# Optimization experiments

Measured on AMD Instinct MI355X. Metric: run time of the kernel, lower is better.

The kernel has to match this reference:

```python
import jax, jax.numpy as jnp
import numpy as np

N_USER = 50000
N_ITEM = 50000
E = 600000
IN_F = 128
HID = 256
OUT = 256
HEADS = 4
D = HID // HEADS
EPS = 1e-5


def setup_inputs() -> dict:
    key = jax.random.key(0)
    ks = jax.random.split(key, 32)
    inp = {}
    inp['x_user'] = jax.random.normal(ks[0], (N_USER, IN_F), jnp.float32)
    inp['x_item'] = jax.random.normal(ks[1], (N_ITEM, IN_F), jnp.float32)
    inp['ui_src'] = jax.random.randint(ks[2], (E,), 0, N_USER)
    inp['ui_dst'] = jax.random.randint(ks[3], (E,), 0, N_ITEM)
    inp['iu_src'] = jax.random.randint(ks[4], (E,), 0, N_ITEM)
    inp['iu_dst'] = jax.random.randint(ks[5], (E,), 0, N_USER)
    dims = [IN_F, HID, HID, HID]
    i = 6
    for l in range(4):
        din = dims[l]
        inp['W%d' % (l + 1)] = jax.random.normal(ks[i], (2, din, HID), jnp.float32) * (1.0 / np.sqrt(din)); i += 1
        inp['al%d' % (l + 1)] = jax.random.normal(ks[i], (2, HEADS, D), jnp.float32) * 0.1; i += 1
        inp['ar%d' % (l + 1)] = jax.random.normal(ks[i], (2, HEADS, D), jnp.float32) * 0.1; i += 1
        inp['b%d' % (l + 1)] = jnp.zeros((2, HID), jnp.float32); i += 1
    inp['bn_g'] = jnp.ones((3, 2, HID), jnp.float32)
    inp['bn_b'] = jnp.zeros((3, 2, HID), jnp.float32)
    return inp


def gat_conv(x_src, x_dst, src, dst, W, al, ar, b, n_dst):
    # DGL GATConv: shared fc, per-head additive attention, segment softmax over dst.
    H, Dh = al.shape
    z_src = (x_src @ W).reshape(-1, H, Dh)   # [Ns,H,D]
    z_dst = (x_dst @ W).reshape(-1, H, Dh)   # [Nd,H,D]
    el = jnp.sum(z_src * al, axis=-1)        # [Ns,H]
    er = jnp.sum(z_dst * ar, axis=-1)        # [Nd,H]
    e = jax.nn.leaky_relu(el[src] + er[dst], 0.2)          # [E,H]
    m = jax.ops.segment_max(e, dst, num_segments=n_dst)    # [Nd,H]
    ex = jnp.exp(e - m[dst])
    s = jax.ops.segment_sum(ex, dst, num_segments=n_dst)
    alpha = ex / s[dst]                                    # [E,H]
    out = jax.ops.segment_sum(z_src[src] * alpha[:, :, None], dst, num_segments=n_dst)
    return out.reshape(n_dst, H * Dh) + b


def batchnorm(x, g, beta):
    mu = jnp.mean(x, axis=0)
    var = jnp.mean((x - mu) ** 2, axis=0)
    return (x - mu) * jax.lax.rsqrt(var + EPS) * g + beta


def _forward(x_user, x_item, ui_src, ui_dst, iu_src, iu_dst,
             W1, al1, ar1, b1, W2, al2, ar2, b2, W3, al3, ar3, b3, W4, al4, ar4, b4,
             bn_g, bn_b):
    def layer(hu, hi, W, al, ar, b):
        h_item = gat_conv(hu, hi, ui_src, ui_dst, W[0], al[0], ar[0], b[0], N_ITEM)
        h_user = gat_conv(hi, hu, iu_src, iu_dst, W[1], al[1], ar[1], b[1], N_USER)
        return h_user, h_item  # mean over single relation per dst type = identity

    hu, hi = layer(x_user, x_item, W1, al1, ar1, b1)
    hu = jax.nn.leaky_relu(batchnorm(hu, bn_g[0, 0], bn_b[0, 0]), 0.01)
    hi = jax.nn.leaky_relu(batchnorm(hi, bn_g[0, 1], bn_b[0, 1]), 0.01)
    hu, hi = layer(hu, hi, W2, al2, ar2, b2)
    hu = jax.nn.leaky_relu(batchnorm(hu, bn_g[1, 0], bn_b[1, 0]), 0.01)
    hi = jax.nn.leaky_relu(batchnorm(hi, bn_g[1, 1], bn_b[1, 1]), 0.01)
    hu, hi = layer(hu, hi, W3, al3, ar3, b3)
    hu = jnp.tanh(batchnorm(hu, bn_g[2, 0], bn_b[2, 0]))
    hi = jnp.tanh(batchnorm(hi, bn_g[2, 1], bn_b[2, 1]))
    hu, hi = layer(hu, hi, W4, al4, ar4, b4)
    return hu.reshape(-1, OUT), hi.reshape(-1, OUT)


def reference(x_user, x_item, ui_src, ui_dst, iu_src, iu_dst,
              W1, al1, ar1, b1, W2, al2, ar2, b2, W3, al3, ar3, b3, W4, al4, ar4, b4,
              bn_g, bn_b):
    return _forward(x_user, x_item, ui_src, ui_dst, iu_src, iu_dst,
                    W1, al1, ar1, b1, W2, al2, ar2, b2, W3, al3, ar3, b3,
                    W4, al4, ar4, b4, bn_g, bn_b)
```

## Files before the change

### kernel.cpp

```cpp
#include <hip/hip_runtime.h>
#include <hip/hip_bf16.h>
#include <type_traits>

#define NN 50000
#define NE 600000
#define HF 256

typedef float f32x4 __attribute__((ext_vector_type(4)));
typedef _Float16 f16x8 __attribute__((ext_vector_type(8)));
typedef _Float16 f16x4 __attribute__((ext_vector_type(4)));

__global__ __launch_bounds__(256) void k_tofp16_2(const float* __restrict__ A,
                                                  const float* __restrict__ B,
                                                  _Float16* __restrict__ OA,
                                                  _Float16* __restrict__ OB, int n4) {
  int i = blockIdx.x * 256 + threadIdx.x;
  const float* X = (i < n4) ? A : B;
  _Float16* Y = (i < n4) ? OA : OB;
  int j = (i < n4) ? i : i - n4;
  if (j < n4) {
    float4 v = reinterpret_cast<const float4*>(X)[j];
    f16x4 o = {(_Float16)v.x, (_Float16)v.y, (_Float16)v.z, (_Float16)v.w};
    reinterpret_cast<f16x4*>(Y)[j] = o;
  }
}

struct TArgs {
  const float* W[8];
  _Float16* dst[8];
  int K[8];
  int cum[9];
};
__global__ __launch_bounds__(256) void k_transpose_all(TArgs t) {
  int idx = blockIdx.x * 256 + threadIdx.x;
#pragma unroll
  for (int s = 0; s < 8; ++s) {
    if (idx >= t.cum[s] && idx < t.cum[s + 1]) {
      int local = idx - t.cum[s];
      int K = t.K[s];
      int k = local >> 8;
      int n = local & 255;
      t.dst[s][(size_t)n * K + k] = (_Float16)t.W[s][local];
    }
  }
}

__global__ __launch_bounds__(256) void k_makeattn_all(
    const float* __restrict__ W1, const float* __restrict__ W2,
    const float* __restrict__ W3, const float* __restrict__ W4,
    const float* __restrict__ ar1, const float* __restrict__ ar2,
    const float* __restrict__ ar3, const float* __restrict__ ar4,
    float* __restrict__ out) {
  int idx = blockIdx.x * 256 + threadIdx.x;
  if (idx >= 8 * 256 * 4) return;
  int h = idx & 3;
  int k = (idx >> 2) & 255;
  int s = idx >> 10;
  int l = s >> 1, r = s & 1;
  int K = (l == 0) ? 128 : 256;
  if (k >= K) return;
  const float* W = (l == 0 ? W1 : l == 1 ? W2 : l == 2 ? W3 : W4) + (size_t)r * K * 256;
  const float* a = (l == 0 ? ar1 : l == 1 ? ar2 : l == 2 ? ar3 : ar4) + r * 256 + h * 64;
  const float* wrow = W + (size_t)k * 256 + h * 64;
  float sum = 0.f;
#pragma unroll 8
  for (int d = 0; d < 64; ++d) sum += wrow[d] * a[d];
  out[s * 1024 + k * 4 + h] = sum;
}

__global__ __launch_bounds__(256) void k_gemv_er2(const _Float16* __restrict__ Xi,
                                                  const _Float16* __restrict__ Xu,
                                                  const float* __restrict__ war0,
                                                  const float* __restrict__ war1,
                                                  float* __restrict__ ER0, float* __restrict__ ER1,
                                                  int K) {
  int nb = (NN + 3) / 4;
  int rel = blockIdx.x >= nb;
  int bid = rel ? blockIdx.x - nb : blockIdx.x;
  const _Float16* X = rel ? Xu : Xi;
  const float* wa = rel ? war1 : war0;
  float* out = rel ? ER1 : ER0;
  int wid = bid * 4 + (threadIdx.x >> 6);
  if (wid >= NN) return;
  int lane = threadIdx.x & 63;
  float p0 = 0.f, p1 = 0.f, p2 = 0.f, p3 = 0.f;
  int k0 = lane * 4;
  if (k0 < K) {
    f16x4 x = *reinterpret_cast<const f16x4*>(X + (size_t)wid * K + k0);
    float xv[4] = {(float)x.x, (float)x.y, (float)x.z, (float)x.w};
#pragma unroll
    for (int j = 0; j < 4; ++j) {
      float4 wv = *reinterpret_cast<const float4*>(wa + (k0 + j) * 4);
      p0 += xv[j] * wv.x; p1 += xv[j] * wv.y; p2 += xv[j] * wv.z; p3 += xv[j] * wv.w;
    }
  }
#pragma unroll
  for (int off = 32; off > 0; off >>= 1) {
    p0 += __shfl_down(p0, off); p1 += __shfl_down(p1, off);
    p2 += __shfl_down(p2, off); p3 += __shfl_down(p3, off);
  }
  if (lane == 0)
    *reinterpret_cast<float4*>(out + (size_t)wid * 4) = (float4){p0, p1, p2, p3};
}

struct GArgs {
  const _Float16* A0; const _Float16* A1;
  const _Float16* Wt0; const _Float16* Wt1;
  _Float16* Z0; _Float16* Z1;
  const float* al0; const float* al1;
  float* EL0; float* EL1;
  int M, K;
};

__global__ __launch_bounds__(256) void k_gemm5(GArgs ga) {
  __shared__ _Float16 As[2][64 * 64];
  const int nrow = (NN + 63) / 64;
  int side = blockIdx.x >= nrow;
  int bid = side ? blockIdx.x - nrow : blockIdx.x;
  const _Float16* A = side ? ga.A1 : ga.A0;
  const _Float16* Wt = side ? ga.Wt1 : ga.Wt0;
  _Float16* Z = side ? ga.Z1 : ga.Z0;
  const float* al = side ? ga.al1 : ga.al0;
  float* EL = side ? ga.EL1 : ga.EL0;
  const int K = ga.K, M = ga.M;
  int row0 = bid * 64;
  int wave = threadIdx.x >> 6;
  int lane = threadIdx.x & 63;
  int lr = lane & 15, kg = lane >> 4;
  int col0 = wave * 64;

  auto stage = [&](int buf, int k0) {
#pragma unroll
    for (int j = 0; j < 2; ++j) {
      int Lb = j * 4096 + wave * 1024;
      int L = Lb + lane * 16;
      int r = L >> 7;
      int kb = (L & 127) ^ ((r & 7) << 4);
      int rg = row0 + r; rg = rg < M ? rg : M - 1;
      const char* gsrc = (const char*)A + ((size_t)rg * K + k0) * 2 + kb;
      char* ldst = (char*)(&As[buf][0]) + Lb;
      __builtin_amdgcn_global_load_lds(
          (const __attribute__((address_space(1))) unsigned int*)gsrc,
          (__attribute__((address_space(3))) unsigned int*)ldst, 16, 0, 0);
    }
  };

  f32x4 acc[4][4];
#pragma unroll
  for (int i = 0; i < 4; ++i)
#pragma unroll
    for (int j = 0; j < 4; ++j) acc[i][j] = (f32x4){0.f, 0.f, 0.f, 0.f};

  int nt = K >> 6;
  stage(0, 0);
  __syncthreads();
  for (int t = 0; t < nt; ++t) {
    if (t + 1 < nt) stage((t + 1) & 1, (t + 1) * 64);
    const char* abuf = (const char*)(&As[t & 1][0]);
#pragma unroll
    for (int s = 0; s < 2; ++s) {
      int kk = t * 64 + s * 32 + kg * 8;
      f16x8 af[4], bfr[4];
#pragma unroll
      for (int mt = 0; mt < 4; ++mt) {
        int r = mt * 16 + lr;
        int cb = ((s << 6) | (kg << 4)) ^ ((r & 7) << 4);
        af[mt] = *reinterpret_cast<const f16x8*>(abuf + r * 128 + cb);
      }
#pragma unroll
      for (int ct = 0; ct < 4; ++ct) {
        int c = col0 + ct * 16 + lr;
        bfr[ct] = *reinterpret_cast<const f16x8*>(Wt + (size_t)c * K + kk);
      }
#pragma unroll
      for (int mt = 0; mt < 4; ++mt)
#pragma unroll
        for (int ct = 0; ct < 4; ++ct)
          acc[mt][ct] = __builtin_amdgcn_mfma_f32_16x16x32_f16(af[mt], bfr[ct], acc[mt][ct], 0, 0, 0);
    }
    __syncthreads();
  }

#pragma unroll
  for (int mt = 0; mt < 4; ++mt) {
#pragma unroll
    for (int r = 0; r < 4; ++r) {
      int row = row0 + mt * 16 + kg * 4 + r;
      if (row < M) {
#pragma unroll
        for (int ct = 0; ct < 4; ++ct) {
          int col = col0 + ct * 16 + lr;
          Z[(size_t)row * HF + col] = (_Float16)acc[mt][ct][r];
        }
      }
    }
  }
  float al4[4];
#pragma unroll
  for (int ct = 0; ct < 4; ++ct) al4[ct] = al[col0 + ct * 16 + lr];
#pragma unroll
  for (int mt = 0; mt < 4; ++mt) {
#pragma unroll
    for (int r = 0; r < 4; ++r) {
      float p = acc[mt][0][r] * al4[0] + acc[mt][1][r] * al4[1] +
                acc[mt][2][r] * al4[2] + acc[mt][3][r] * al4[3];
#pragma unroll
      for (int off = 1; off < 16; off <<= 1) p += __shfl_xor(p, off);
      int row = row0 + mt * 16 + kg * 4 + r;
      if (lr == 0 && row < M) EL[(size_t)row * 4 + wave] = p;
    }
  }
}

__global__ __launch_bounds__(256) void k_hist2(const int* __restrict__ d0, const int* __restrict__ d1,
                                               int* __restrict__ c0, int* __restrict__ c1) {
  int t = blockIdx.x * 256 + threadIdx.x;
  if (t < NE) atomicAdd(&c0[d0[t]], 1);
  else if (t < 2 * NE) atomicAdd(&c1[d1[t - NE]], 1);
}

__global__ __launch_bounds__(1024) void k_scan1_2(const int* __restrict__ c0, const int* __restrict__ c1,
                                                  int* __restrict__ rp0, int* __restrict__ rp1,
                                                  int* __restrict__ b0, int* __restrict__ b1, int nscan) {
  __shared__ int tmp[1024];
  int rel = blockIdx.x >= nscan;
  int blk = rel ? blockIdx.x - nscan : blockIdx.x;
  const int* counts = rel ? c1 : c0;
  int* rp = rel ? rp1 : rp0;
  int* bsum = rel ? b1 : b0;
  int i = blk * 1024 + threadIdx.x;
  int v = (i < NN) ? counts[i] : 0;
  tmp[threadIdx.x] = v;
  __syncthreads();
  for (int off = 1; off < 1024; off <<= 1) {
    int t = (threadIdx.x >= off) ? tmp[threadIdx.x - off] : 0;
    __syncthreads();
    tmp[threadIdx.x] += t;
    __syncthreads();
  }
  if (i < NN) rp[i] = tmp[threadIdx.x] - v;
  if (threadIdx.x == 1023) bsum[blk] = tmp[1023];
}

__global__ __launch_bounds__(128) void k_scan2_2(int* __restrict__ b0, int* __restrict__ b1, int nb) {
  int rel = threadIdx.x >> 6;
  int l = threadIdx.x & 63;
  int* bsum = rel ? b1 : b0;
  int orig = (l < nb) ? bsum[l] : 0;
  int v = orig;
#pragma unroll
  for (int off = 1; off < 64; off <<= 1) {
    int t = __shfl_up(v, off);
    if (l >= off) v += t;
  }
  if (l < nb) bsum[l] = v - orig;
}

__global__ __launch_bounds__(1024) void k_scan3_2(int* __restrict__ rp0, int* __restrict__ rp1,
                                                  const int* __restrict__ b0, const int* __restrict__ b1,
                                                  int nscan) {
  int rel = blockIdx.x >= nscan;
  int blk = rel ? blockIdx.x - nscan : blockIdx.x;
  int* rp = rel ? rp1 : rp0;
  const int* bsum = rel ? b1 : b0;
  int i = blk * 1024 + threadIdx.x;
  if (i < NN) rp[i] += bsum[blk];
  if (i == 0) rp[NN] = NE;
}

__global__ __launch_bounds__(256) void k_scatter2(
    const int* __restrict__ s0, const int* __restrict__ d0,
    const int* __restrict__ s1, const int* __restrict__ d1,
    const int* __restrict__ rp0, const int* __restrict__ rp1,
    int* __restrict__ f0, int* __restrict__ f1,
    int* __restrict__ cs0, int* __restrict__ cs1) {
  int t = blockIdx.x * 256 + threadIdx.x;
  if (t < NE) {
    int d = d0[t];
    int pos = rp0[d] + atomicAdd(&f0[d], 1);
    cs0[pos] = s0[t];
  } else if (t < 2 * NE) {
    int e = t - NE;
    int d = d1[e];
    int pos = rp1[d] + atomicAdd(&f1[d], 1);
    cs1[pos] = s1[e];
  }
}

__device__ __forceinline__ float pick_h(float4 v, int h) {
  float r = v.x;
  r = (h == 1) ? v.y : r;
  r = (h == 2) ? v.z : r;
  r = (h == 3) ? v.w : r;
  return r;
}

template <typename OT>
__global__ __launch_bounds__(256) void k_agg2(
    const int* __restrict__ rpA, const int* __restrict__ csA,
    const float* __restrict__ elA, const float* __restrict__ erA,
    const _Float16* __restrict__ ZA, const float* __restrict__ bA, OT* __restrict__ oA,
    const int* __restrict__ rpB, const int* __restrict__ csB,
    const float* __restrict__ elB, const float* __restrict__ erB,
    const _Float16* __restrict__ ZB, const float* __restrict__ bB, OT* __restrict__ oB) {
  __shared__ float exs[4][256];
  __shared__ int ssrc[4][64];
  int nb = (NN + 3) / 4;
  int rel = blockIdx.x >= nb;
  int bid = rel ? blockIdx.x - nb : blockIdx.x;
  const int* rp = rel ? rpB : rpA;
  const int* csrc = rel ? csB : csA;
  const float* el = rel ? elB : elA;
  const float* er = rel ? erB : erA;
  const _Float16* Z = rel ? ZB : ZA;
  const float* bias = rel ? bB : bA;
  OT* out = rel ? oB : oA;

  int wv = threadIdx.x >> 6;
  int wid = bid * 4 + wv;
  if (wid >= NN) return;
  int lane = threadIdx.x & 63;
  int half = lane >> 5, l5 = lane & 31;
  int c0 = l5 * 8;
  int h = l5 >> 3;
  int beg = rp[wid], end = rp[wid + 1];
  int deg = end - beg;

  if (deg == 0) {
    if (half == 0) {
      float4 b0 = *reinterpret_cast<const float4*>(bias + c0);
      float4 b1 = *reinterpret_cast<const float4*>(bias + c0 + 4);
      if constexpr (std::is_same<OT, float>::value) {
        float4* op = reinterpret_cast<float4*>(out + (size_t)wid * HF + c0);
        op[0] = b0; op[1] = b1;
      } else {
        f16x8 o = {(_Float16)b0.x, (_Float16)b0.y, (_Float16)b0.z, (_Float16)b0.w,
                   (_Float16)b1.x, (_Float16)b1.y, (_Float16)b1.z, (_Float16)b1.w};
        *reinterpret_cast<f16x8*>(out + (size_t)wid * HF + c0) = o;
      }
    }
    return;
  }

  if (deg <= 64) {
    int s = 0;
    float4 x = {-1e30f, -1e30f, -1e30f, -1e30f};
    float4 b = *reinterpret_cast<const float4*>(er + (size_t)wid * 4);
    if (lane < deg) {
      s = csrc[beg + lane];
      float4 a = reinterpret_cast<const float4*>(el)[s];
      x.x = a.x + b.x; x.x = x.x >= 0.f ? x.x : 0.2f * x.x;
      x.y = a.y + b.y; x.y = x.y >= 0.f ? x.y : 0.2f * x.y;
      x.z = a.z + b.z; x.z = x.z >= 0.f ? x.z : 0.2f * x.z;
      x.w = a.w + b.w; x.w = x.w >= 0.f ? x.w : 0.2f * x.w;
    }
    float4 m = x;
#pragma unroll
    for (int off = 32; off > 0; off >>= 1) {
      m.x = fmaxf(m.x, __shfl_xor(m.x, off));
      m.y = fmaxf(m.y, __shfl_xor(m.y, off));
      m.z = fmaxf(m.z, __shfl_xor(m.z, off));
      m.w = fmaxf(m.w, __shfl_xor(m.w, off));
    }
    float4 ex = {0.f, 0.f, 0.f, 0.f};
    if (lane < deg) {
      ex.x = __expf(x.x - m.x);
      ex.y = __expf(x.y - m.y);
      ex.z = __expf(x.z - m.z);
      ex.w = __expf(x.w - m.w);
    }
    float4 sm = ex;
#pragma unroll
    for (int off = 32; off > 0; off >>= 1) {
      sm.x += __shfl_xor(sm.x, off);
      sm.y += __shfl_xor(sm.y, off);
      sm.z += __shfl_xor(sm.z, off);
      sm.w += __shfl_xor(sm.w, off);
    }
    float inv = 1.0f / pick_h(sm, h);
    if (lane < deg) {
      *reinterpret_cast<float4*>(&exs[wv][lane * 4]) = ex;
      ssrc[wv][lane] = s;
    }
    float a8[8] = {0.f, 0.f, 0.f, 0.f, 0.f, 0.f, 0.f, 0.f};
    int j = half;
#define AGG_STEP(J)                                                        \
    {                                                                      \
      int sj = ssrc[wv][(J)];                                              \
      float wj = exs[wv][(J) * 4 + h];                                     \
      f16x8 z = *reinterpret_cast<const f16x8*>(Z + (size_t)sj * HF + c0); \
      _Pragma("unroll")                                                    \
      for (int q = 0; q < 8; ++q) a8[q] += wj * (float)z[q];               \
    }
    for (; j + 6 < deg; j += 8) {
      AGG_STEP(j); AGG_STEP(j + 2); AGG_STEP(j + 4); AGG_STEP(j + 6);
    }
    for (; j < deg; j += 2) { AGG_STEP(j); }
#undef AGG_STEP
#pragma unroll
    for (int q = 0; q < 8; ++q) a8[q] += __shfl_xor(a8[q], 32);
    if (half == 0) {
      float4 b0 = *reinterpret_cast<const float4*>(bias + c0);
      float4 b1 = *reinterpret_cast<const float4*>(bias + c0 + 4);
      float r0 = a8[0] * inv + b0.x, r1 = a8[1] * inv + b0.y;
      float r2 = a8[2] * inv + b0.z, r3 = a8[3] * inv + b0.w;
      float r4 = a8[4] * inv + b1.x, r5 = a8[5] * inv + b1.y;
      float r6 = a8[6] * inv + b1.z, r7 = a8[7] * inv + b1.w;
      if constexpr (std::is_same<OT, float>::value) {
        float4* op = reinterpret_cast<float4*>(out + (size_t)wid * HF + c0);
        op[0] = (float4){r0, r1, r2, r3};
        op[1] = (float4){r4, r5, r6, r7};
      } else {
        f16x8 o = {(_Float16)r0, (_Float16)r1, (_Float16)r2, (_Float16)r3,
                   (_Float16)r4, (_Float16)r5, (_Float16)r6, (_Float16)r7};
        *reinterpret_cast<f16x8*>(out + (size_t)wid * HF + c0) = o;
      }
    }
    return;
  }

  {
    int c4 = lane * 4;
    int h4 = lane >> 4;
    float4 b = *reinterpret_cast<const float4*>(er + (size_t)wid * 4);
    float4 m = {-1e30f, -1e30f, -1e30f, -1e30f};
    for (int e = beg; e < end; ++e) {
      int s = csrc[e];
      float4 a = reinterpret_cast<const float4*>(el)[s];
      float4 x;
      x.x = a.x + b.x; x.x = x.x >= 0.f ? x.x : 0.2f * x.x;
      x.y = a.y + b.y; x.y = x.y >= 0.f ? x.y : 0.2f * x.y;
      x.z = a.z + b.z; x.z = x.z >= 0.f ? x.z : 0.2f * x.z;
      x.w = a.w + b.w; x.w = x.w >= 0.f ? x.w : 0.2f * x.w;
      m.x = fmaxf(m.x, x.x); m.y = fmaxf(m.y, x.y);
      m.z = fmaxf(m.z, x.z); m.w = fmaxf(m.w, x.w);
    }
    float4 sm = {0.f, 0.f, 0.f, 0.f};
    float4 acc = {0.f, 0.f, 0.f, 0.f};
    for (int e = beg; e < end; ++e) {
      int s = csrc[e];
      float4 a = reinterpret_cast<const float4*>(el)[s];
      float4 x;
      x.x = a.x + b.x; x.x = x.x >= 0.f ? x.x : 0.2f * x.x;
      x.y = a.y + b.y; x.y = x.y >= 0.f ? x.y : 0.2f * x.y;
      x.z = a.z + b.z; x.z = x.z >= 0.f ? x.z : 0.2f * x.z;
      x.w = a.w + b.w; x.w = x.w >= 0.f ? x.w : 0.2f * x.w;
      float4 exv;
      exv.x = __expf(x.x - m.x); exv.y = __expf(x.y - m.y);
      exv.z = __expf(x.z - m.z); exv.w = __expf(x.w - m.w);
      sm.x += exv.x; sm.y += exv.y; sm.z += exv.z; sm.w += exv.w;
      float w0 = pick_h(exv, h4);
      f16x4 z0 = *reinterpret_cast<const f16x4*>(Z + (size_t)s * HF + c4);
      acc.x += w0 * (float)z0.x;
      acc.y += w0 * (float)z0.y;
      acc.z += w0 * (float)z0.z;
      acc.w += w0 * (float)z0.w;
    }
    float inv = 1.0f / pick_h(sm, h4);
    float4 bv = *reinterpret_cast<const float4*>(bias + c4);
    float r0 = acc.x * inv + bv.x, r1 = acc.y * inv + bv.y;
    float r2 = acc.z * inv + bv.z, r3 = acc.w * inv + bv.w;
    if constexpr (std::is_same<OT, float>::value) {
      *reinterpret_cast<float4*>(out + (size_t)wid * HF + c4) = (float4){r0, r1, r2, r3};
    } else {
      f16x4 o = {(_Float16)r0, (_Float16)r1, (_Float16)r2, (_Float16)r3};
      *reinterpret_cast<f16x4*>(out + (size_t)wid * HF + c4) = o;
    }
  }
}

__global__ __launch_bounds__(256) void k_bn_stats2(const _Float16* __restrict__ XU,
                                                   const _Float16* __restrict__ XI,
                                                   float* __restrict__ su, float* __restrict__ qu,
                                                   float* __restrict__ si, float* __restrict__ qi) {
  int rel = blockIdx.x >> 9;
  int blk = blockIdx.x & 511;
  const _Float16* X = rel ? XI : XU;
  float* sums = rel ? si : su;
  float* sqs = rel ? qi : qu;
  int c = threadIdx.x;
  float s = 0.f, q = 0.f;
  for (int r = blk; r < NN; r += 512) {
    float v = (float)X[(size_t)r * HF + c];
    s += v;
    q += v * v;
  }
  atomicAdd(&sums[c], s);
  atomicAdd(&sqs[c], q);
}

__global__ __launch_bounds__(256) void k_bn_apply2(
    const _Float16* __restrict__ XU, const _Float16* __restrict__ XI,
    const float* __restrict__ su, const float* __restrict__ qu,
    const float* __restrict__ si, const float* __restrict__ qi,
    const float* __restrict__ gU, const float* __restrict__ btU,
    const float* __restrict__ gI, const float* __restrict__ btI,
    _Float16* __restrict__ YU, _Float16* __restrict__ YI, int act) {
  const int nb = NN * HF / 8 / 256;
  int rel = blockIdx.x >= nb;
  int bid = rel ? blockIdx.x - nb : blockIdx.x;
  const _Float16* X = rel ? XI : XU;
  const float* sums = rel ? si : su;
  const float* sqs = rel ? qi : qu;
  const float* g = rel ? gI : gU;
  const float* bt = rel ? btI : btU;
  _Float16* Y = rel ? YI : YU;
  int gid = bid * 256 + threadIdx.x;
  int i0 = gid * 8;
  int c0 = i0 & 255;
  const float invN = 1.0f / NN;
  f16x8 xv = *reinterpret_cast<const f16x8*>(X + i0);
  float4 s0 = *reinterpret_cast<const float4*>(sums + c0);
  float4 s1 = *reinterpret_cast<const float4*>(sums + c0 + 4);
  float4 q0 = *reinterpret_cast<const float4*>(sqs + c0);
  float4 q1 = *reinterpret_cast<const float4*>(sqs + c0 + 4);
  float4 g0 = *reinterpret_cast<const float4*>(g + c0);
  float4 g1 = *reinterpret_cast<const float4*>(g + c0 + 4);
  float4 b0 = *reinterpret_cast<const float4*>(bt + c0);
  float4 b1 = *reinterpret_cast<const float4*>(bt + c0 + 4);
  float sa[8] = {s0.x, s0.y, s0.z, s0.w, s1.x, s1.y, s1.z, s1.w};
  float qa[8] = {q0.x, q0.y, q0.z, q0.w, q1.x, q1.y, q1.z, q1.w};
  float ga[8] = {g0.x, g0.y, g0.z, g0.w, g1.x, g1.y, g1.z, g1.w};
  float ba[8] = {b0.x, b0.y, b0.z, b0.w, b1.x, b1.y, b1.z, b1.w};
  f16x8 o;
#pragma unroll
  for (int j = 0; j < 8; ++j) {
    float mu = sa[j] * invN;
    float var = qa[j] * invN - mu * mu;
    float sc = rsqrtf(var + 1e-5f) * ga[j];
    float v = ((float)xv[j] - mu) * sc + ba[j];
    v = act ? tanhf(v) : (v >= 0.f ? v : 0.01f * v);
    o[j] = (_Float16)v;
  }
  *reinterpret_cast<f16x8*>(Y + i0) = o;
}

extern "C" void kernel_launch(void* const* d_in, const int* in_sizes, int n_in,
                              void* d_out, int out_size, void* d_ws, size_t ws_size,
                              hipStream_t stream) {
  (void)in_sizes; (void)n_in; (void)out_size; (void)ws_size;
  const float* x_user = (const float*)d_in[0];
  const float* x_item = (const float*)d_in[1];
  const int* ui_src = (const int*)d_in[2];
  const int* ui_dst = (const int*)d_in[3];
  const int* iu_src = (const int*)d_in[4];
  const int* iu_dst = (const int*)d_in[5];
  const float *Wp[4], *alp[4], *arp[4], *bp[4];
  for (int l = 0; l < 4; ++l) {
    Wp[l]  = (const float*)d_in[6 + 4 * l];
    alp[l] = (const float*)d_in[7 + 4 * l];
    arp[l] = (const float*)d_in[8 + 4 * l];
    bp[l]  = (const float*)d_in[9 + 4 * l];
  }
  const float* bng = (const float*)d_in[22];
  const float* bnb = (const float*)d_in[23];

  char* w = (char*)d_ws;
  auto alloc = [&](size_t bytes) -> void* {
    void* p = (void*)w;
    w += (bytes + 255) & ~(size_t)255;
    return p;
  };
  _Float16* XU16 = (_Float16*)alloc((size_t)NN * 128 * 2);
  _Float16* XI16 = (_Float16*)alloc((size_t)NN * 128 * 2);
  _Float16* H16U = (_Float16*)alloc((size_t)NN * HF * 2);
  _Float16* H16I = (_Float16*)alloc((size_t)NN * HF * 2);
  _Float16* Z0 = (_Float16*)alloc((size_t)NN * HF * 2);
  _Float16* Z1 = (_Float16*)alloc((size_t)NN * HF * 2);
  _Float16* RAW16U = (_Float16*)alloc((size_t)NN * HF * 2);
  _Float16* RAW16I = (_Float16*)alloc((size_t)NN * HF * 2);
  float* EL0 = (float*)alloc((size_t)NN * 4 * 4);
  float* ER0 = (float*)alloc((size_t)NN * 4 * 4);
  float* EL1 = (float*)alloc((size_t)NN * 4 * 4);
  float* ER1 = (float*)alloc((size_t)NN * 4 * 4);
  _Float16* WT = (_Float16*)alloc((size_t)8 * 65536 * 2);
  float* ATTN = (float*)alloc((size_t)8 * 1024 * 4);
  int* rp_ui = (int*)alloc((size_t)(NN + 1) * 4);
  int* rp_iu = (int*)alloc((size_t)(NN + 1) * 4);
  int* csrc_ui = (int*)alloc((size_t)NE * 4);
  int* csrc_iu = (int*)alloc((size_t)NE * 4);
  int* counts = (int*)alloc((size_t)4 * NN * 4);
  int* bsum_ui = (int*)alloc((size_t)64 * 4);
  int* bsum_iu = (int*)alloc((size_t)64 * 4);
  float* stats = (float*)alloc((size_t)6 * 512 * 4);

  int* counts_ui = counts;
  int* counts_iu = counts + NN;
  int* fill_ui = counts + 2 * NN;
  int* fill_iu = counts + 3 * NN;

  hipMemsetAsync(counts, 0, (size_t)4 * NN * 4, stream);
  hipMemsetAsync(stats, 0, (size_t)6 * 512 * 4, stream);

  int n4 = NN * 128 / 4;
  k_tofp16_2<<<(2 * n4 + 255) / 256, 256, 0, stream>>>(x_user, x_item, XU16, XI16, n4);

  TArgs ta;
  int cum = 0;
  for (int l = 0; l < 4; ++l) {
    int K = (l == 0) ? 128 : 256;
    for (int r = 0; r < 2; ++r) {
      int s = l * 2 + r;
      ta.W[s] = Wp[l] + (size_t)r * K * HF;
      ta.dst[s] = WT + (size_t)s * 65536;
      ta.K[s] = K;
      ta.cum[s] = cum;
      cum += K * 256;
    }
  }
  ta.cum[8] = cum;
  k_transpose_all<<<(cum + 255) / 256, 256, 0, stream>>>(ta);

  k_makeattn_all<<<(8 * 256 * 4 + 255) / 256, 256, 0, stream>>>(
      Wp[0], Wp[1], Wp[2], Wp[3], arp[0], arp[1], arp[2], arp[3], ATTN);

  int egrid2 = (2 * NE + 255) / 256;
  int nscan = (NN + 1023) / 1024;
  k_hist2<<<egrid2, 256, 0, stream>>>(ui_dst, iu_dst, counts_ui, counts_iu);
  k_scan1_2<<<2 * nscan, 1024, 0, stream>>>(counts_ui, counts_iu, rp_ui, rp_iu, bsum_ui, bsum_iu, nscan);
  k_scan2_2<<<1, 128, 0, stream>>>(bsum_ui, bsum_iu, nscan);
  k_scan3_2<<<2 * nscan, 1024, 0, stream>>>(rp_ui, rp_iu, bsum_ui, bsum_iu, nscan);
  k_scatter2<<<egrid2, 256, 0, stream>>>(ui_src, ui_dst, iu_src, iu_dst, rp_ui, rp_iu,
                                         fill_ui, fill_iu, csrc_ui, csrc_iu);

  int agrid = (NN + 3) / 4;
  int nrow = (NN + 63) / 64;
  float* out_user = (float*)d_out;
  float* out_item = (float*)d_out + (size_t)NN * HF;

  for (int l = 0; l < 4; ++l) {
    int K = (l == 0) ? 128 : 256;
    const _Float16* Au = (l == 0) ? XU16 : H16U;
    const _Float16* Ai = (l == 0) ? XI16 : H16I;
    const float* war0 = ATTN + (size_t)(l * 2 + 0) * 1024;
    const float* war1 = ATTN + (size_t)(l * 2 + 1) * 1024;

    k_gemv_er2<<<2 * agrid, 256, 0, stream>>>(Ai, Au, war0, war1, ER0, ER1, K);

    GArgs ga;
    ga.A0 = Au; ga.A1 = Ai;
    ga.Wt0 = WT + (size_t)(l * 2 + 0) * 65536;
    ga.Wt1 = WT + (size_t)(l * 2 + 1) * 65536;
    ga.Z0 = Z0; ga.Z1 = Z1;
    ga.al0 = alp[l] + 0; ga.al1 = alp[l] + 256;
    ga.EL0 = EL0; ga.EL1 = EL1;
    ga.M = NN; ga.K = K;
    k_gemm5<<<2 * nrow, 256, 0, stream>>>(ga);

    if (l < 3)
      k_agg2<_Float16><<<2 * agrid, 256, 0, stream>>>(
          rp_ui, csrc_ui, EL0, ER0, Z0, bp[l] + 0, RAW16I,
          rp_iu, csrc_iu, EL1, ER1, Z1, bp[l] + 256, RAW16U);
    else
      k_agg2<float><<<2 * agrid, 256, 0, stream>>>(
          rp_ui, csrc_ui, EL0, ER0, Z0, bp[l] + 0, out_item,
          rp_iu, csrc_iu, EL1, ER1, Z1, bp[l] + 256, out_user);

    if (l < 3) {
      int act = (l == 2) ? 1 : 0;
      float* su = stats + (size_t)(l * 2 + 0) * 512;
      float* si = stats + (size_t)(l * 2 + 1) * 512;
      k_bn_stats2<<<1024, 256, 0, stream>>>(RAW16U, RAW16I, su, su + 256, si, si + 256);
      k_bn_apply2<<<2 * (NN * HF / 8 / 256), 256, 0, stream>>>(
          RAW16U, RAW16I, su, su + 256, si, si + 256,
          bng + (size_t)(l * 2 + 0) * 256, bnb + (size_t)(l * 2 + 0) * 256,
          bng + (size_t)(l * 2 + 1) * 256, bnb + (size_t)(l * 2 + 1) * 256,
          H16U, H16I, act);
    }
  }
}
```

Measured before the change: 1.048 ms.

## Fuse ER projection into GEMM via MFMA and degree-sort aggregation rows

Removes the separate k_gemv_er2 pass by computing the destination attention scores ER inside k_gemm5. Wave 0 runs extra MFMAs against a folded W·ar matrix stored as fp16, using the A tiles already staged in LDS, which saves a full re-read of the node features each layer. It also builds a per-relation permutation that sorts destination nodes by in-degree, so the aggregation waves in each block see similar edge counts and diverge less. The cost is extra MFMA work on one wave of the GEMM, fp16 rounding of the folded attention weights, a few new preprocessing kernels, and scattered output rows in aggregation.

```diff
diff --git a/kernel.cpp b/kernel.cpp
--- a/kernel.cpp
+++ b/kernel.cpp
@@ -50,7 +50,7 @@
     const float* __restrict__ W3, const float* __restrict__ W4,
     const float* __restrict__ ar1, const float* __restrict__ ar2,
     const float* __restrict__ ar3, const float* __restrict__ ar4,
-    float* __restrict__ out) {
+    _Float16* __restrict__ wart) {
   int idx = blockIdx.x * 256 + threadIdx.x;
   if (idx >= 8 * 256 * 4) return;
   int h = idx & 3;
@@ -65,42 +65,7 @@
   float sum = 0.f;
 #pragma unroll 8
   for (int d = 0; d < 64; ++d) sum += wrow[d] * a[d];
-  out[s * 1024 + k * 4 + h] = sum;
-}
-
-__global__ __launch_bounds__(256) void k_gemv_er2(const _Float16* __restrict__ Xi,
-                                                  const _Float16* __restrict__ Xu,
-                                                  const float* __restrict__ war0,
-                                                  const float* __restrict__ war1,
-                                                  float* __restrict__ ER0, float* __restrict__ ER1,
-                                                  int K) {
-  int nb = (NN + 3) / 4;
-  int rel = blockIdx.x >= nb;
-  int bid = rel ? blockIdx.x - nb : blockIdx.x;
-  const _Float16* X = rel ? Xu : Xi;
-  const float* wa = rel ? war1 : war0;
-  float* out = rel ? ER1 : ER0;
-  int wid = bid * 4 + (threadIdx.x >> 6);
-  if (wid >= NN) return;
-  int lane = threadIdx.x & 63;
-  float p0 = 0.f, p1 = 0.f, p2 = 0.f, p3 = 0.f;
-  int k0 = lane * 4;
-  if (k0 < K) {
-    f16x4 x = *reinterpret_cast<const f16x4*>(X + (size_t)wid * K + k0);
-    float xv[4] = {(float)x.x, (float)x.y, (float)x.z, (float)x.w};
-#pragma unroll
-    for (int j = 0; j < 4; ++j) {
-      float4 wv = *reinterpret_cast<const float4*>(wa + (k0 + j) * 4);
-      p0 += xv[j] * wv.x; p1 += xv[j] * wv.y; p2 += xv[j] * wv.z; p3 += xv[j] * wv.w;
-    }
-  }
-#pragma unroll
-  for (int off = 32; off > 0; off >>= 1) {
-    p0 += __shfl_down(p0, off); p1 += __shfl_down(p1, off);
-    p2 += __shfl_down(p2, off); p3 += __shfl_down(p3, off);
-  }
-  if (lane == 0)
-    *reinterpret_cast<float4*>(out + (size_t)wid * 4) = (float4){p0, p1, p2, p3};
+  wart[(size_t)s * 4096 + h * 256 + k] = (_Float16)sum;
 }
 
 struct GArgs {
@@ -109,6 +74,8 @@
   _Float16* Z0; _Float16* Z1;
   const float* al0; const float* al1;
   float* EL0; float* EL1;
+  const _Float16* wart_s0; const _Float16* wart_s1;
+  float* ER_s0; float* ER_s1;
   int M, K;
 };
 
@@ -122,6 +89,8 @@
   _Float16* Z = side ? ga.Z1 : ga.Z0;
   const float* al = side ? ga.al1 : ga.al0;
   float* EL = side ? ga.EL1 : ga.EL0;
+  const _Float16* wart = side ? ga.wart_s1 : ga.wart_s0;
+  float* ER = side ? ga.ER_s1 : ga.ER_s0;
   const int K = ga.K, M = ga.M;
   int row0 = bid * 64;
   int wave = threadIdx.x >> 6;
@@ -150,6 +119,9 @@
   for (int i = 0; i < 4; ++i)
 #pragma unroll
     for (int j = 0; j < 4; ++j) acc[i][j] = (f32x4){0.f, 0.f, 0.f, 0.f};
+  f32x4 acc_er[4];
+#pragma unroll
+  for (int i = 0; i < 4; ++i) acc_er[i] = (f32x4){0.f, 0.f, 0.f, 0.f};
 
   int nt = K >> 6;
   stage(0, 0);
@@ -177,6 +149,12 @@
 #pragma unroll
         for (int ct = 0; ct < 4; ++ct)
           acc[mt][ct] = __builtin_amdgcn_mfma_f32_16x16x32_f16(af[mt], bfr[ct], acc[mt][ct], 0, 0, 0);
+      if (wave == 0) {
+        f16x8 eb = *reinterpret_cast<const f16x8*>(wart + lr * 256 + kk);
+#pragma unroll
+        for (int mt = 0; mt < 4; ++mt)
+          acc_er[mt] = __builtin_amdgcn_mfma_f32_16x16x32_f16(af[mt], eb, acc_er[mt], 0, 0, 0);
+      }
     }
     __syncthreads();
   }
@@ -208,6 +186,16 @@
       for (int off = 1; off < 16; off <<= 1) p += __shfl_xor(p, off);
       int row = row0 + mt * 16 + kg * 4 + r;
       if (lr == 0 && row < M) EL[(size_t)row * 4 + wave] = p;
+    }
+  }
+  if (wave == 0 && lr < 4) {
+#pragma unroll
+    for (int mt = 0; mt < 4; ++mt) {
+#pragma unroll
+      for (int r = 0; r < 4; ++r) {
+        int row = row0 + mt * 16 + kg * 4 + r;
+        if (row < M) ER[(size_t)row * 4 + lr] = acc_er[mt][r];
+      }
     }
   }
 }
@@ -287,6 +275,52 @@
   }
 }
 
+__global__ __launch_bounds__(256) void k_deghist2(const int* __restrict__ rp0,
+                                                  const int* __restrict__ rp1,
+                                                  int* __restrict__ dh) {
+  int t = blockIdx.x * 256 + threadIdx.x;
+  if (t < NN) {
+    int d = rp0[t + 1] - rp0[t];
+    atomicAdd(&dh[min(d, 63)], 1);
+  } else if (t < 2 * NN) {
+    int n = t - NN;
+    int d = rp1[n + 1] - rp1[n];
+    atomicAdd(&dh[64 + min(d, 63)], 1);
+  }
+}
+
+__global__ __launch_bounds__(128) void k_degscan(const int* __restrict__ dh, int* __restrict__ dofs) {
+  int rel = threadIdx.x >> 6;
+  int l = threadIdx.x & 63;
+  int orig = dh[rel * 64 + l];
+  int v = orig;
+#pragma unroll
+  for (int off = 1; off < 64; off <<= 1) {
+    int t = __shfl_up(v, off);
+    if (l >= off) v += t;
+  }
+  dofs[rel * 64 + l] = v - orig;
+}
+
+__global__ __launch_bounds__(256) void k_permscatter2(const int* __restrict__ rp0,
+                                                      const int* __restrict__ rp1,
+                                                      const int* __restrict__ dofs,
+                                                      int* __restrict__ dfill,
+                                                      int* __restrict__ perm0,
+                                                      int* __restrict__ perm1) {
+  int t = blockIdx.x * 256 + threadIdx.x;
+  if (t < NN) {
+    int b = min(rp0[t + 1] - rp0[t], 63);
+    int pos = dofs[b] + atomicAdd(&dfill[b], 1);
+    perm0[pos] = t;
+  } else if (t < 2 * NN) {
+    int n = t - NN;
+    int b = min(rp1[n + 1] - rp1[n], 63);
+    int pos = dofs[64 + b] + atomicAdd(&dfill[64 + b], 1);
+    perm1[pos] = n;
+  }
+}
+
 __device__ __forceinline__ float pick_h(float4 v, int h) {
   float r = v.x;
   r = (h == 1) ? v.y : r;
@@ -297,10 +331,10 @@
 
 template <typename OT>
 __global__ __launch_bounds__(256) void k_agg2(
-    const int* __restrict__ rpA, const int* __restrict__ csA,
+    const int* __restrict__ rpA, const int* __restrict__ csA, const int* __restrict__ permA,
     const float* __restrict__ elA, const float* __restrict__ erA,
     const _Float16* __restrict__ ZA, const float* __restrict__ bA, OT* __restrict__ oA,
-    const int* __restrict__ rpB, const int* __restrict__ csB,
+    const int* __restrict__ rpB, const int* __restrict__ csB, const int* __restrict__ permB,
     const float* __restrict__ elB, const float* __restrict__ erB,
     const _Float16* __restrict__ ZB, const float* __restrict__ bB, OT* __restrict__ oB) {
   __shared__ float exs[4][256];
@@ -317,8 +351,9 @@
   OT* out = rel ? oB : oA;
 
   int wv = threadIdx.x >> 6;
-  int wid = bid * 4 + wv;
-  if (wid >= NN) return;
+  int gid = bid * 4 + wv;
+  if (gid >= NN) return;
+  int wid = (rel ? permB : permA)[gid];
   int lane = threadIdx.x & 63;
   int half = lane >> 5, l5 = lane & 31;
   int c0 = l5 * 8;
@@ -574,23 +609,31 @@
   float* EL1 = (float*)alloc((size_t)NN * 4 * 4);
   float* ER1 = (float*)alloc((size_t)NN * 4 * 4);
   _Float16* WT = (_Float16*)alloc((size_t)8 * 65536 * 2);
-  float* ATTN = (float*)alloc((size_t)8 * 1024 * 4);
+  _Float16* WART = (_Float16*)alloc((size_t)8 * 4096 * 2);
   int* rp_ui = (int*)alloc((size_t)(NN + 1) * 4);
   int* rp_iu = (int*)alloc((size_t)(NN + 1) * 4);
   int* csrc_ui = (int*)alloc((size_t)NE * 4);
   int* csrc_iu = (int*)alloc((size_t)NE * 4);
+  int* perm_ui = (int*)alloc((size_t)NN * 4);
+  int* perm_iu = (int*)alloc((size_t)NN * 4);
   int* counts = (int*)alloc((size_t)4 * NN * 4);
   int* bsum_ui = (int*)alloc((size_t)64 * 4);
   int* bsum_iu = (int*)alloc((size_t)64 * 4);
+  int* degws = (int*)alloc((size_t)384 * 4);
   float* stats = (float*)alloc((size_t)6 * 512 * 4);
 
   int* counts_ui = counts;
   int* counts_iu = counts + NN;
   int* fill_ui = counts + 2 * NN;
   int* fill_iu = counts + 3 * NN;
+  int* dh = degws;
+  int* dofs = degws + 128;
+  int* dfill = degws + 256;
 
   hipMemsetAsync(counts, 0, (size_t)4 * NN * 4, stream);
   hipMemsetAsync(stats, 0, (size_t)6 * 512 * 4, stream);
+  hipMemsetAsync(WART, 0, (size_t)8 * 4096 * 2, stream);
+  hipMemsetAsync(degws, 0, (size_t)384 * 4, stream);
 
   int n4 = NN * 128 / 4;
   k_tofp16_2<<<(2 * n4 + 255) / 256, 256, 0, stream>>>(x_user, x_item, XU16, XI16, n4);
@@ -612,7 +655,7 @@
   k_transpose_all<<<(cum + 255) / 256, 256, 0, stream>>>(ta);
 
   k_makeattn_all<<<(8 * 256 * 4 + 255) / 256, 256, 0, stream>>>(
-      Wp[0], Wp[1], Wp[2], Wp[3], arp[0], arp[1], arp[2], arp[3], ATTN);
+      Wp[0], Wp[1], Wp[2], Wp[3], arp[0], arp[1], arp[2], arp[3], WART);
 
   int egrid2 = (2 * NE + 255) / 256;
   int nscan = (NN + 1023) / 1024;
@@ -623,6 +666,11 @@
   k_scatter2<<<egrid2, 256, 0, stream>>>(ui_src, ui_dst, iu_src, iu_dst, rp_ui, rp_iu,
                                          fill_ui, fill_iu, csrc_ui, csrc_iu);
 
+  int ngrid2 = (2 * NN + 255) / 256;
+  k_deghist2<<<ngrid2, 256, 0, stream>>>(rp_ui, rp_iu, dh);
+  k_degscan<<<1, 128, 0, stream>>>(dh, dofs);
+  k_permscatter2<<<ngrid2, 256, 0, stream>>>(rp_ui, rp_iu, dofs, dfill, perm_ui, perm_iu);
+
   int agrid = (NN + 3) / 4;
   int nrow = (NN + 63) / 64;
   float* out_user = (float*)d_out;
@@ -632,10 +680,6 @@
     int K = (l == 0) ? 128 : 256;
     const _Float16* Au = (l == 0) ? XU16 : H16U;
     const _Float16* Ai = (l == 0) ? XI16 : H16I;
-    const float* war0 = ATTN + (size_t)(l * 2 + 0) * 1024;
-    const float* war1 = ATTN + (size_t)(l * 2 + 1) * 1024;
-
-    k_gemv_er2<<<2 * agrid, 256, 0, stream>>>(Ai, Au, war0, war1, ER0, ER1, K);
 
     GArgs ga;
     ga.A0 = Au; ga.A1 = Ai;
@@ -644,17 +688,20 @@
     ga.Z0 = Z0; ga.Z1 = Z1;
     ga.al0 = alp[l] + 0; ga.al1 = alp[l] + 256;
     ga.EL0 = EL0; ga.EL1 = EL1;
+    ga.wart_s0 = WART + (size_t)(l * 2 + 1) * 4096;
+    ga.wart_s1 = WART + (size_t)(l * 2 + 0) * 4096;
+    ga.ER_s0 = ER1; ga.ER_s1 = ER0;
     ga.M = NN; ga.K = K;
     k_gemm5<<<2 * nrow, 256, 0, stream>>>(ga);
 
     if (l < 3)
       k_agg2<_Float16><<<2 * agrid, 256, 0, stream>>>(
-          rp_ui, csrc_ui, EL0, ER0, Z0, bp[l] + 0, RAW16I,
-          rp_iu, csrc_iu, EL1, ER1, Z1, bp[l] + 256, RAW16U);
+          rp_ui, csrc_ui, perm_ui, EL0, ER0, Z0, bp[l] + 0, RAW16I,
+          rp_iu, csrc_iu, perm_iu, EL1, ER1, Z1, bp[l] + 256, RAW16U);
     else
       k_agg2<float><<<2 * agrid, 256, 0, stream>>>(
-          rp_ui, csrc_ui, EL0, ER0, Z0, bp[l] + 0, out_item,
-          rp_iu, csrc_iu, EL1, ER1, Z1, bp[l] + 256, out_user);
+          rp_ui, csrc_ui, perm_ui, EL0, ER0, Z0, bp[l] + 0, out_item,
+          rp_iu, csrc_iu, perm_iu, EL1, ER1, Z1, bp[l] + 256, out_user);
 
     if (l < 3) {
       int act = (l == 2) ? 1 : 0;
```

New measurement: 1.339 ms. +27.7%, slower.
